# Kernel optimization log

Measured on AMD Instinct MI355X. Metric: run time of the kernel, lower is better.

## Reference

```python
import jax, jax.numpy as jnp
import numpy as np

B, T, D, E, C = 2, 2048, 2048, 8, 512
O1 = D // E  # per-expert hidden width (out_features // num_experts)


def setup_inputs() -> dict:
    key = jax.random.key(0)
    k = jax.random.split(key, 8)
    s = 1.0 / np.sqrt(D)
    return {
        "x": jax.random.normal(k[0], (B, T, D), dtype=jnp.float32),
        "dispatch_mask": jax.random.uniform(k[1], (B, T, E, C), dtype=jnp.float32),
        "combine_array": jax.random.uniform(k[2], (B, T, E, C), dtype=jnp.float32),
        # contract weights: nn.Linear(D, D) reshaped to (E, D//E, D)
        "W1": jax.random.uniform(k[3], (E, O1, D), jnp.float32, -s, s),
        "b1": jax.random.uniform(k[4], (E, O1), jnp.float32, -s, s),
        # expand weights: nn.Linear(D, D) reshaped to (E, D, D//E)
        "W2": jax.random.uniform(k[5], (E, D, O1), jnp.float32, -s, s),
        "b2": jax.random.uniform(k[6], (D,), jnp.float32, -s, s),
    }


def reference(x, dispatch_mask, combine_array, W1, b1, W2, b2):
    # --- ExpertsChooseMaskedContract ---
    # einsum('btd,btec,eod->beco') split into two GEMM-shaped contractions
    xe = jnp.einsum('btd,btec->becd', x, dispatch_mask)          # [B,E,C,D]
    h = jnp.einsum('becd,eod->beco', xe, W1) + b1[None, :, None, :]  # [B,E,C,O1]
    # --- GELU (torch nn.GELU default = exact erf form) ---
    h = jax.nn.gelu(h, approximate=False)
    # --- ExpertsChooseMaskedExpand (homogeneous-coords bias == add b2 then combine) ---
    y = jnp.einsum('beci,eoi->beco', h, W2) + b2[None, None, None, :]  # [B,E,C,D]
    out = jnp.einsum('beco,btec->bto', y, combine_array)          # [B,T,D]
    return out
```

## Files before the change

kernel.cpp:

```cpp
#include <hip/hip_runtime.h>
#include <math.h>

#define BB 2
#define TT 2048
#define DD 2048
#define EE 8
#define CCv 512
#define OO1 256

typedef unsigned short u16;
typedef __bf16 bf16x8 __attribute__((ext_vector_type(8)));
typedef float f32x4 __attribute__((ext_vector_type(4)));

__device__ __forceinline__ u16 f2bf(float f) {
    unsigned u = __float_as_uint(f);
    unsigned r = (u + 0x7fffu + ((u >> 16) & 1u)) >> 16;
    return (u16)r;
}

__device__ __forceinline__ void gload16(const void* g, void* s) {
    __builtin_amdgcn_global_load_lds(
        (const __attribute__((address_space(1))) void*)g,
        (__attribute__((address_space(3))) void*)s, 16, 0, 0);
}

__global__ __launch_bounds__(256) void conv_cast(const float* __restrict__ in,
                                                 u16* __restrict__ out, long n) {
    long i = ((long)blockIdx.x * 256 + threadIdx.x) * 4;
    float4 v = *(const float4*)&in[i];
    ushort4 o; o.x = f2bf(v.x); o.y = f2bf(v.y); o.z = f2bf(v.z); o.w = f2bf(v.w);
    *(ushort4*)&out[i] = o;
}

__global__ __launch_bounds__(256) void transpose_conv(
    const float* __restrict__ in, long inHi, long inLo, int modZ, long sIn,
    u16* __restrict__ out, long outZ, long sOut)
{
    __shared__ float tile[32][33];
    const int z = blockIdx.z;
    const float* ib = in + (long)(z / modZ) * inHi + (long)(z % modZ) * inLo;
    u16* ob = out + (long)z * outZ;
    const int t0 = blockIdx.y * 32, c0 = blockIdx.x * 32;
    const int tid = threadIdx.x;
    const int r = tid >> 3, c4 = (tid & 7) * 4;

    float4 v = *(const float4*)&ib[(long)(t0 + r) * sIn + c0 + c4];
    tile[r][c4 + 0] = v.x; tile[r][c4 + 1] = v.y;
    tile[r][c4 + 2] = v.z; tile[r][c4 + 3] = v.w;
    __syncthreads();

    const int oc = tid >> 3, t4 = (tid & 7) * 4;
    ushort4 o;
    o.x = f2bf(tile[t4 + 0][oc]);
    o.y = f2bf(tile[t4 + 1][oc]);
    o.z = f2bf(tile[t4 + 2][oc]);
    o.w = f2bf(tile[t4 + 3][oc]);
    *(ushort4*)&ob[(long)(c0 + oc) * sOut + t0 + t4] = o;
}

template<int EPI>
__global__ __launch_bounds__(256)
void mfma_gemm(const u16* __restrict__ A, long ldA, long aHi, long aLo, int modA,
               const u16* __restrict__ B, long ldB, long bHi, long bLo, int modB,
               void* __restrict__ Cout, long ldC, long cHi, long cLo, int modC,
               const float* __restrict__ bias, long biasLo, int modBias,
               int M, int N, int K)
{
    __shared__ __align__(16) char smem[32768];
    char* smA = smem;
    char* smB = smem + 16384;

    const int z = blockIdx.z;
    const char* Ab = (const char*)(A + (long)(z / modA) * aHi + (long)(z % modA) * aLo);
    const char* Bb = (const char*)(B + (long)(z / modB) * bHi + (long)(z % modB) * bLo);
    const long ldAb = ldA * 2, ldBb = ldB * 2;

    const int m0 = blockIdx.y * 128, n0 = blockIdx.x * 128;
    const int tid = threadIdx.x;
    const int l = tid & 63;
    const int w = tid >> 6;
    const int wm = w >> 1, wn = w & 1;

    const int srow = l >> 3;
    const int schunk = (l & 7) ^ srow;
    const int frow = l & 15;
    const int fgrp = l >> 4;
    const int fch0 = fgrp ^ (l & 7);

    int aoff[4], boff[4];
#pragma unroll
    for (int i = 0; i < 4; ++i) {
        aoff[i] = (wm * 64 + i * 16 + frow) * 128 + fch0 * 16;
        boff[i] = (wn * 64 + i * 16 + frow) * 128 + fch0 * 16;
    }

    f32x4 acc[4][4];
    const f32x4 zero4 = {0.f, 0.f, 0.f, 0.f};
#pragma unroll
    for (int i = 0; i < 4; ++i)
#pragma unroll
        for (int j = 0; j < 4; ++j) acc[i][j] = zero4;

    const long sgo = (long)schunk * 16;

    for (int k0 = 0; k0 < K; k0 += 64) {
        const long kb = (long)k0 * 2;
#pragma unroll
        for (int j = 0; j < 4; ++j) {
            const int rr = (j * 4 + w) * 8 + srow;
            gload16(Ab + (long)(m0 + rr) * ldAb + kb + sgo, smA + (j * 4 + w) * 1024);
            gload16(Bb + (long)(n0 + rr) * ldBb + kb + sgo, smB + (j * 4 + w) * 1024);
        }
        __syncthreads();
#pragma unroll
        for (int kk = 0; kk < 2; ++kk) {
            const int kx = kk * 64;
            bf16x8 af[4], bfr[4];
#pragma unroll
            for (int i = 0; i < 4; ++i) af[i] = *(const bf16x8*)(smA + (aoff[i] ^ kx));
#pragma unroll
            for (int i = 0; i < 4; ++i) bfr[i] = *(const bf16x8*)(smB + (boff[i] ^ kx));
#pragma unroll
            for (int mi = 0; mi < 4; ++mi)
#pragma unroll
                for (int ni = 0; ni < 4; ++ni)
                    acc[mi][ni] = __builtin_amdgcn_mfma_f32_16x16x32_bf16(
                        af[mi], bfr[ni], acc[mi][ni], 0, 0, 0);
        }
        __syncthreads();
    }

    const long cbase = (long)(z / modC) * cHi + (long)(z % modC) * cLo;
    const float* biasB = bias + (long)(z % modBias) * biasLo;
#pragma unroll
    for (int mi = 0; mi < 4; ++mi) {
#pragma unroll
        for (int ni = 0; ni < 4; ++ni) {
            const int col = n0 + wn * 64 + ni * 16 + frow;
            const int rowb = m0 + wm * 64 + mi * 16 + fgrp * 4;
#pragma unroll
            for (int r = 0; r < 4; ++r) {
                float v = acc[mi][ni][r];
                const int row = rowb + r;
                if (EPI == 1) {
                    v += biasB[col];
                    v = 0.5f * v * (1.0f + erff(v * 0.70710678118654752f));
                } else {
                    v += biasB[row];
                }
                ((u16*)Cout)[cbase + (long)row * ldC + col] = f2bf(v);
            }
        }
    }
}

template<int OUTBF>
__global__ __launch_bounds__(512, 2)
void mfma_gemm_256(const u16* __restrict__ A, long ldA, long aHi, long aLo, int modA,
                   const u16* __restrict__ B, long ldB, long bHi, long bLo, int modB,
                   void* __restrict__ Cout, long ldC, long cHi, long cLo, int modC,
                   int M, int N, int K)
{
    __shared__ __align__(16) char smem[131072];

    const int z = blockIdx.z;
    const char* Ab = (const char*)(A + (long)(z / modA) * aHi + (long)(z % modA) * aLo);
    const char* Bb = (const char*)(B + (long)(z / modB) * bHi + (long)(z % modB) * bLo);
    const long ldAb = ldA * 2, ldBb = ldB * 2;

    const int m0 = blockIdx.y * 256, n0 = blockIdx.x * 256;
    const int tid = threadIdx.x;
    const int l = tid & 63;
    const int w = tid >> 6;
    const int wm = w >> 2, wn = w & 3;

    const int srow = l >> 3;
    const int schunk = (l & 7) ^ srow;
    const long sgo = (long)schunk * 16;
    const int frow = l & 15, fgrp = l >> 4;
    const int cs0 = (fgrp ^ (l & 7)) * 16;

    auto stage = [&](int kt, int bsel, int half, int j) {
        const int rr = (w * 2 + j) * 8 + srow;
        const char* gb = (half < 2) ? Ab : Bb;
        const long ld = (half < 2) ? ldAb : ldBb;
        const int gr = ((half < 2) ? m0 + half * 128 : n0 + (half - 2) * 128) + rr;
        gload16(gb + (long)gr * ld + (long)kt * 128 + sgo,
                smem + bsel * 65536 + half * 16384 + (w * 2 + j) * 1024);
    };

    f32x4 acc[2][4][2][2];
    const f32x4 zero4 = {0.f, 0.f, 0.f, 0.f};
#pragma unroll
    for (int qm = 0; qm < 2; ++qm)
#pragma unroll
        for (int mi = 0; mi < 4; ++mi)
#pragma unroll
            for (int qn = 0; qn < 2; ++qn)
#pragma unroll
                for (int ni = 0; ni < 2; ++ni) acc[qm][mi][qn][ni] = zero4;

    int aoff[4], boff[2];
#pragma unroll
    for (int mi = 0; mi < 4; ++mi) aoff[mi] = (wm * 64 + mi * 16 + frow) * 128 + cs0;
#pragma unroll
    for (int ni = 0; ni < 2; ++ni) boff[ni] = (wn * 32 + ni * 16 + frow) * 128 + cs0;

    stage(0, 0, 0, 0); stage(0, 0, 0, 1);
    stage(0, 0, 2, 0); stage(0, 0, 2, 1);
    stage(0, 0, 3, 0); stage(0, 0, 3, 1);
    stage(0, 0, 1, 0); stage(0, 0, 1, 1);
    asm volatile("s_waitcnt vmcnt(4)" ::: "memory");
    __builtin_amdgcn_s_barrier();

    const int NT = K >> 6;
    for (int kt = 0; kt < NT; ++kt) {
        const char* buf = smem + (kt & 1) * 65536;
        const int sb = (kt & 1) ^ 1;
        const bool pf = (kt + 1) < NT;
        const int kn = kt + 1;
        bf16x8 af[4][2], bq0[2][2], bq1[2][2];

#pragma unroll
        for (int mi = 0; mi < 4; ++mi) {
            af[mi][0] = *(const bf16x8*)(buf + aoff[mi]);
            af[mi][1] = *(const bf16x8*)(buf + (aoff[mi] ^ 64));
        }
#pragma unroll
        for (int ni = 0; ni < 2; ++ni) {
            bq0[ni][0] = *(const bf16x8*)(buf + 32768 + boff[ni]);
            bq0[ni][1] = *(const bf16x8*)(buf + 32768 + (boff[ni] ^ 64));
        }
        if (pf) { stage(kn, sb, 0, 0); stage(kn, sb, 0, 1); }
        if (pf) { asm volatile("s_waitcnt vmcnt(4)" ::: "memory"); }
        else    { asm volatile("s_waitcnt vmcnt(2)" ::: "memory"); }
        __builtin_amdgcn_s_barrier();
        asm volatile("s_waitcnt lgkmcnt(0)" ::: "memory");
        __builtin_amdgcn_sched_barrier(0);
        __builtin_amdgcn_s_setprio(1);
#pragma unroll
        for (int kk = 0; kk < 2; ++kk)
#pragma unroll
            for (int mi = 0; mi < 4; ++mi)
#pragma unroll
                for (int ni = 0; ni < 2; ++ni)
                    acc[0][mi][0][ni] = __builtin_amdgcn_mfma_f32_16x16x32_bf16(
                        af[mi][kk], bq0[ni][kk], acc[0][mi][0][ni], 0, 0, 0);
        __builtin_amdgcn_s_setprio(0);

#pragma unroll
        for (int ni = 0; ni < 2; ++ni) {
            bq1[ni][0] = *(const bf16x8*)(buf + 49152 + boff[ni]);
            bq1[ni][1] = *(const bf16x8*)(buf + 49152 + (boff[ni] ^ 64));
        }
        if (pf) { stage(kn, sb, 2, 0); stage(kn, sb, 2, 1); }
        if (pf) { asm volatile("s_waitcnt vmcnt(4)" ::: "memory"); }
        else    { asm volatile("s_waitcnt vmcnt(0)" ::: "memory"); }
        __builtin_amdgcn_s_barrier();
        asm volatile("s_waitcnt lgkmcnt(0)" ::: "memory");
        __builtin_amdgcn_sched_barrier(0);
        __builtin_amdgcn_s_setprio(1);
#pragma unroll
        for (int kk = 0; kk < 2; ++kk)
#pragma unroll
            for (int mi = 0; mi < 4; ++mi)
#pragma unroll
                for (int ni = 0; ni < 2; ++ni)
                    acc[0][mi][1][ni] = __builtin_amdgcn_mfma_f32_16x16x32_bf16(
                        af[mi][kk], bq1[ni][kk], acc[0][mi][1][ni], 0, 0, 0);
        __builtin_amdgcn_s_setprio(0);

#pragma unroll
        for (int mi = 0; mi < 4; ++mi) {
            af[mi][0] = *(const bf16x8*)(buf + 16384 + aoff[mi]);
            af[mi][1] = *(const bf16x8*)(buf + 16384 + (aoff[mi] ^ 64));
        }
        if (pf) { stage(kn, sb, 3, 0); stage(kn, sb, 3, 1); }
        asm volatile("s_waitcnt lgkmcnt(0)" ::: "memory");
        __builtin_amdgcn_sched_barrier(0);
        __builtin_amdgcn_s_setprio(1);
#pragma unroll
        for (int kk = 0; kk < 2; ++kk)
#pragma unroll
            for (int mi = 0; mi < 4; ++mi)
#pragma unroll
                for (int ni = 0; ni < 2; ++ni)
                    acc[1][mi][1][ni] = __builtin_amdgcn_mfma_f32_16x16x32_bf16(
                        af[mi][kk], bq1[ni][kk], acc[1][mi][1][ni], 0, 0, 0);
        __builtin_amdgcn_s_setprio(0);

        if (pf) { stage(kn, sb, 1, 0); stage(kn, sb, 1, 1); }
        if (pf) { asm volatile("s_waitcnt vmcnt(4)" ::: "memory"); }
        __builtin_amdgcn_s_barrier();
        __builtin_amdgcn_s_setprio(1);
#pragma unroll
        for (int kk = 0; kk < 2; ++kk)
#pragma unroll
            for (int mi = 0; mi < 4; ++mi)
#pragma unroll
                for (int ni = 0; ni < 2; ++ni)
                    acc[1][mi][0][ni] = __builtin_amdgcn_mfma_f32_16x16x32_bf16(
                        af[mi][kk], bq0[ni][kk], acc[1][mi][0][ni], 0, 0, 0);
        __builtin_amdgcn_s_setprio(0);
    }

    const long cbase = (long)(z / modC) * cHi + (long)(z % modC) * cLo;
#pragma unroll
    for (int qm = 0; qm < 2; ++qm)
#pragma unroll
        for (int mi = 0; mi < 4; ++mi)
#pragma unroll
            for (int qn = 0; qn < 2; ++qn)
#pragma unroll
                for (int ni = 0; ni < 2; ++ni) {
                    const int col = n0 + qn * 128 + wn * 32 + ni * 16 + frow;
                    const int rowb = m0 + qm * 128 + wm * 64 + mi * 16 + fgrp * 4;
#pragma unroll
                    for (int r = 0; r < 4; ++r) {
                        const float v = acc[qm][mi][qn][ni][r];
                        const long idx = cbase + (long)(rowb + r) * ldC + col;
                        if (OUTBF) ((u16*)Cout)[idx] = f2bf(v);
                        else       ((float*)Cout)[idx] = v;
                    }
                }
}

template<int OUTBF>
__global__ __launch_bounds__(512, 2)
void mfma_gemm_big(const u16* __restrict__ A, long ldA, long aHi, long aLo, int modA,
                   const u16* __restrict__ B, long ldB, long bHi, long bLo, int modB,
                   void* __restrict__ Cout, long ldC, long cHi, long cLo, int modC,
                   int M, int N, int K)
{
    __shared__ __align__(16) char smem[147456];

    const int z = blockIdx.z;
    const char* Ab = (const char*)(A + (long)(z / modA) * aHi + (long)(z % modA) * aLo);
    const char* Bb = (const char*)(B + (long)(z / modB) * bHi + (long)(z % modB) * bLo);
    const long ldAb = ldA * 2, ldBb = ldB * 2;

    const int m0 = blockIdx.y * 256, n0 = blockIdx.x * 128;
    const int tid = threadIdx.x;
    const int l = tid & 63;
    const int w = tid >> 6;
    const int wm = w >> 1, wn = w & 1;

    const int srow = l >> 3;
    const int schunk = (l & 7) ^ srow;
    const long sgo = (long)schunk * 16;
    const int frow = l & 15;
    const int fgrp = l >> 4;
    const int fsw = (fgrp ^ (l & 7)) * 16;

    auto stageA = [&](int kt, int bsel, int j) {
        const int rr = (j * 8 + w) * 8 + srow;
        gload16(Ab + (long)(m0 + rr) * ldAb + (long)kt * 128 + sgo,
                smem + bsel * 49152 + (j * 8 + w) * 1024);
    };
    auto stageB = [&](int kt, int bsel, int j) {
        const int rr = (j * 8 + w) * 8 + srow;
        gload16(Bb + (long)(n0 + rr) * ldBb + (long)kt * 128 + sgo,
                smem + bsel * 49152 + 32768 + (j * 8 + w) * 1024);
    };

    f32x4 acc[4][4];
    const f32x4 zero4 = {0.f, 0.f, 0.f, 0.f};
#pragma unroll
    for (int i = 0; i < 4; ++i)
#pragma unroll
        for (int j = 0; j < 4; ++j) acc[i][j] = zero4;

    int aoff[4], boff[4];
#pragma unroll
    for (int i = 0; i < 4; ++i) {
        aoff[i] = (wm * 64 + i * 16 + frow) * 128 + fsw;
        boff[i] = (wn * 64 + i * 16 + frow) * 128 + fsw;
    }

#pragma unroll
    for (int j = 0; j < 4; ++j) stageA(0, 0, j);
#pragma unroll
    for (int j = 0; j < 2; ++j) stageB(0, 0, j);
#pragma unroll
    for (int j = 0; j < 4; ++j) stageA(1, 1, j);
#pragma unroll
    for (int j = 0; j < 2; ++j) stageB(1, 1, j);
    asm volatile("s_waitcnt vmcnt(6)" ::: "memory");
    __builtin_amdgcn_s_barrier();

    const int NT = K >> 6;
    int bc = 0;
    int sc = 2;
    for (int kt = 0; kt < NT; ++kt) {
        const char* bufA = smem + bc * 49152;
        const char* bufB = bufA + 32768;
        const bool pf = (kt + 2) < NT;
        const int kpf = kt + 2;

        if (pf) {
            stageA(kpf, sc, 0); stageA(kpf, sc, 1);
            stageA(kpf, sc, 2); stageA(kpf, sc, 3);
            stageB(kpf, sc, 0); stageB(kpf, sc, 1);
        }

        bf16x8 af[4][2], bfr[4][2];
#pragma unroll
        for (int mi = 0; mi < 4; ++mi) {
            af[mi][0] = *(const bf16x8*)(bufA + aoff[mi]);
            af[mi][1] = *(const bf16x8*)(bufA + (aoff[mi] ^ 64));
        }
#pragma unroll
        for (int ni = 0; ni < 4; ++ni) {
            bfr[ni][0] = *(const bf16x8*)(bufB + boff[ni]);
            bfr[ni][1] = *(const bf16x8*)(bufB + (boff[ni] ^ 64));
        }

        __builtin_amdgcn_s_setprio(1);
#pragma unroll
        for (int kk = 0; kk < 2; ++kk)
#pragma unroll
            for (int mi = 0; mi < 4; ++mi)
#pragma unroll
                for (int ni = 0; ni < 4; ++ni)
                    acc[mi][ni] = __builtin_amdgcn_mfma_f32_16x16x32_bf16(
                        af[mi][kk], bfr[ni][kk], acc[mi][ni], 0, 0, 0);
        __builtin_amdgcn_s_setprio(0);

        if (pf) { asm volatile("s_waitcnt vmcnt(6)" ::: "memory"); }
        else    { asm volatile("s_waitcnt vmcnt(0)" ::: "memory"); }
        __builtin_amdgcn_s_barrier();

        bc = (bc == 2) ? 0 : bc + 1;
        sc = (sc == 2) ? 0 : sc + 1;
    }

    const long cbase = (long)(z / modC) * cHi + (long)(z % modC) * cLo;
#pragma unroll
    for (int mi = 0; mi < 4; ++mi) {
#pragma unroll
        for (int ni = 0; ni < 4; ++ni) {
            const int col = n0 + wn * 64 + ni * 16 + frow;
            const int rowb = m0 + wm * 64 + mi * 16 + fgrp * 4;
#pragma unroll
            for (int r = 0; r < 4; ++r) {
                const float v = acc[mi][ni][r];
                const long idx = cbase + (long)(rowb + r) * ldC + col;
                if (OUTBF) ((u16*)Cout)[idx] = f2bf(v);
                else       ((float*)Cout)[idx] = v;
            }
        }
    }
}

extern "C" void kernel_launch(void* const* d_in, const int* in_sizes, int n_in,
                              void* d_out, int out_size, void* d_ws, size_t ws_size,
                              hipStream_t stream) {
    const float* x    = (const float*)d_in[0];
    const float* mask = (const float*)d_in[1];
    const float* comb = (const float*)d_in[2];
    const float* W1   = (const float*)d_in[3];
    const float* b1   = (const float*)d_in[4];
    const float* W2   = (const float*)d_in[5];
    const float* b2   = (const float*)d_in[6];
    float* out = (float*)d_out;

    char* ws = (char*)d_ws;
    u16* buf0 = (u16*)ws;
    u16* xT   = (u16*)(ws + 33554432);
    u16* W1b  = (u16*)(ws + 50331648);
    u16* W2b  = (u16*)(ws + 58720256);
    u16* xe   = (u16*)(ws + 67108864);
    u16* h    = (u16*)(ws + 100663296);
    u16* yT   = xe;

    transpose_conv<<<dim3(DD / 32, TT / 32, BB), 256, 0, stream>>>(
        x, (long)TT * DD, 0L, 1, (long)DD, xT, (long)DD * TT, (long)TT);
    transpose_conv<<<dim3(CCv / 32, TT / 32, BB * EE), 256, 0, stream>>>(
        mask, (long)TT * EE * CCv, (long)CCv, EE, (long)EE * CCv,
        buf0, (long)CCv * TT, (long)TT);
    conv_cast<<<(int)((8L * OO1 * DD) / 1024), 256, 0, stream>>>(W1, W1b, 8L * OO1 * DD);
    conv_cast<<<(int)((8L * DD * OO1) / 1024), 256, 0, stream>>>(W2, W2b, 8L * DD * OO1);

    mfma_gemm_256<1><<<dim3(DD / 256, CCv / 256, 16), 512, 0, stream>>>(
        buf0, 2048, 1048576L, 0L, 1,
        xT,   2048, 4194304L, 0L, 8,
        xe,   2048, 1048576L, 0L, 1,
        CCv, DD, TT);

    conv_cast<<<(int)((2L * TT * EE * CCv) / 1024), 256, 0, stream>>>(
        comb, buf0, 2L * TT * EE * CCv);

    mfma_gemm<1><<<dim3(OO1 / 128, CCv / 128, 16), 256, 0, stream>>>(
        xe,  2048, 1048576L, 0L, 1,
        W1b, 2048, 0L, 524288L, 8,
        h,   256, 131072L, 0L, 1,
        b1, 256L, 8, CCv, OO1, DD);

    mfma_gemm<3><<<dim3(CCv / 128, DD / 128, 16), 256, 0, stream>>>(
        W2b, 256, 0L, 524288L, 8,
        h,   256, 131072L, 0L, 1,
        yT,  4096, 8388608L, 512L, 8,
        b2, 0L, 1, DD, CCv, OO1);

    mfma_gemm_big<0><<<dim3(DD / 128, TT / 256, BB), 512, 0, stream>>>(
        buf0, 4096, 8388608L, 0L, 1,
        yT,   4096, 8388608L, 0L, 1,
        out,  2048, 4194304L, 0L, 1,
        TT, DD, EE * CCv);
}
```

Measured before the change: 266.4 us.

## Replace final combine GEMM with split-K 256-tile GEMM plus reduction add

New measurement: 276.7 us. 3.8% more time.

```diff
diff --git a/kernel.cpp b/kernel.cpp
--- a/kernel.cpp
+++ b/kernel.cpp
@@ -30,6 +30,15 @@
     float4 v = *(const float4*)&in[i];
     ushort4 o; o.x = f2bf(v.x); o.y = f2bf(v.y); o.z = f2bf(v.z); o.w = f2bf(v.w);
     *(ushort4*)&out[i] = o;
+}
+
+__global__ __launch_bounds__(256) void add_inplace(float* __restrict__ out,
+                                                   const float* __restrict__ part) {
+    long i = ((long)blockIdx.x * 256 + threadIdx.x) * 4;
+    float4 a = *(float4*)&out[i];
+    float4 b = *(const float4*)&part[i];
+    a.x += b.x; a.y += b.y; a.z += b.z; a.w += b.w;
+    *(float4*)&out[i] = a;
 }
 
 __global__ __launch_bounds__(256) void transpose_conv(
@@ -210,15 +219,24 @@
     stage(0, 0, 2, 0); stage(0, 0, 2, 1);
     stage(0, 0, 3, 0); stage(0, 0, 3, 1);
     stage(0, 0, 1, 0); stage(0, 0, 1, 1);
-    asm volatile("s_waitcnt vmcnt(4)" ::: "memory");
-    __builtin_amdgcn_s_barrier();
 
     const int NT = K >> 6;
     for (int kt = 0; kt < NT; ++kt) {
         const char* buf = smem + (kt & 1) * 65536;
         const int sb = (kt & 1) ^ 1;
         const bool pf = (kt + 1) < NT;
-        const int kn = kt + 1;
+
+        asm volatile("s_waitcnt vmcnt(0)" ::: "memory");
+        __builtin_amdgcn_s_barrier();
+
+        if (pf) {
+            const int kn = kt + 1;
+            stage(kn, sb, 0, 0); stage(kn, sb, 0, 1);
+            stage(kn, sb, 2, 0); stage(kn, sb, 2, 1);
+            stage(kn, sb, 3, 0); stage(kn, sb, 3, 1);
+            stage(kn, sb, 1, 0); stage(kn, sb, 1, 1);
+        }
+
         bf16x8 af[4][2], bq0[2][2], bq1[2][2];
 
 #pragma unroll
@@ -231,10 +249,6 @@
             bq0[ni][0] = *(const bf16x8*)(buf + 32768 + boff[ni]);
             bq0[ni][1] = *(const bf16x8*)(buf + 32768 + (boff[ni] ^ 64));
         }
-        if (pf) { stage(kn, sb, 0, 0); stage(kn, sb, 0, 1); }
-        if (pf) { asm volatile("s_waitcnt vmcnt(4)" ::: "memory"); }
-        else    { asm volatile("s_waitcnt vmcnt(2)" ::: "memory"); }
-        __builtin_amdgcn_s_barrier();
         asm volatile("s_waitcnt lgkmcnt(0)" ::: "memory");
         __builtin_amdgcn_sched_barrier(0);
         __builtin_amdgcn_s_setprio(1);
@@ -253,10 +267,6 @@
             bq1[ni][0] = *(const bf16x8*)(buf + 49152 + boff[ni]);
             bq1[ni][1] = *(const bf16x8*)(buf + 49152 + (boff[ni] ^ 64));
         }
-        if (pf) { stage(kn, sb, 2, 0); stage(kn, sb, 2, 1); }
-        if (pf) { asm volatile("s_waitcnt vmcnt(4)" ::: "memory"); }
-        else    { asm volatile("s_waitcnt vmcnt(0)" ::: "memory"); }
-        __builtin_amdgcn_s_barrier();
         asm volatile("s_waitcnt lgkmcnt(0)" ::: "memory");
         __builtin_amdgcn_sched_barrier(0);
         __builtin_amdgcn_s_setprio(1);
@@ -275,7 +285,6 @@
             af[mi][0] = *(const bf16x8*)(buf + 16384 + aoff[mi]);
             af[mi][1] = *(const bf16x8*)(buf + 16384 + (aoff[mi] ^ 64));
         }
-        if (pf) { stage(kn, sb, 3, 0); stage(kn, sb, 3, 1); }
         asm volatile("s_waitcnt lgkmcnt(0)" ::: "memory");
         __builtin_amdgcn_sched_barrier(0);
         __builtin_amdgcn_s_setprio(1);
@@ -289,9 +298,6 @@
                         af[mi][kk], bq1[ni][kk], acc[1][mi][1][ni], 0, 0, 0);
         __builtin_amdgcn_s_setprio(0);
 
-        if (pf) { stage(kn, sb, 1, 0); stage(kn, sb, 1, 1); }
-        if (pf) { asm volatile("s_waitcnt vmcnt(4)" ::: "memory"); }
-        __builtin_amdgcn_s_barrier();
         __builtin_amdgcn_s_setprio(1);
 #pragma unroll
         for (int kk = 0; kk < 2; ++kk)
@@ -323,133 +329,6 @@
                         else       ((float*)Cout)[idx] = v;
                     }
                 }
-}
-
-template<int OUTBF>
-__global__ __launch_bounds__(512, 2)
-void mfma_gemm_big(const u16* __restrict__ A, long ldA, long aHi, long aLo, int modA,
-                   const u16* __restrict__ B, long ldB, long bHi, long bLo, int modB,
-                   void* __restrict__ Cout, long ldC, long cHi, long cLo, int modC,
-                   int M, int N, int K)
-{
-    __shared__ __align__(16) char smem[147456];
-
-    const int z = blockIdx.z;
-    const char* Ab = (const char*)(A + (long)(z / modA) * aHi + (long)(z % modA) * aLo);
-    const char* Bb = (const char*)(B + (long)(z / modB) * bHi + (long)(z % modB) * bLo);
-    const long ldAb = ldA * 2, ldBb = ldB * 2;
-
-    const int m0 = blockIdx.y * 256, n0 = blockIdx.x * 128;
-    const int tid = threadIdx.x;
-    const int l = tid & 63;
-    const int w = tid >> 6;
-    const int wm = w >> 1, wn = w & 1;
-
-    const int srow = l >> 3;
-    const int schunk = (l & 7) ^ srow;
-    const long sgo = (long)schunk * 16;
-    const int frow = l & 15;
-    const int fgrp = l >> 4;
-    const int fsw = (fgrp ^ (l & 7)) * 16;
-
-    auto stageA = [&](int kt, int bsel, int j) {
-        const int rr = (j * 8 + w) * 8 + srow;
-        gload16(Ab + (long)(m0 + rr) * ldAb + (long)kt * 128 + sgo,
-                smem + bsel * 49152 + (j * 8 + w) * 1024);
-    };
-    auto stageB = [&](int kt, int bsel, int j) {
-        const int rr = (j * 8 + w) * 8 + srow;
-        gload16(Bb + (long)(n0 + rr) * ldBb + (long)kt * 128 + sgo,
-                smem + bsel * 49152 + 32768 + (j * 8 + w) * 1024);
-    };
-
-    f32x4 acc[4][4];
-    const f32x4 zero4 = {0.f, 0.f, 0.f, 0.f};
-#pragma unroll
-    for (int i = 0; i < 4; ++i)
-#pragma unroll
-        for (int j = 0; j < 4; ++j) acc[i][j] = zero4;
-
-    int aoff[4], boff[4];
-#pragma unroll
-    for (int i = 0; i < 4; ++i) {
-        aoff[i] = (wm * 64 + i * 16 + frow) * 128 + fsw;
-        boff[i] = (wn * 64 + i * 16 + frow) * 128 + fsw;
-    }
-
-#pragma unroll
-    for (int j = 0; j < 4; ++j) stageA(0, 0, j);
-#pragma unroll
-    for (int j = 0; j < 2; ++j) stageB(0, 0, j);
-#pragma unroll
-    for (int j = 0; j < 4; ++j) stageA(1, 1, j);
-#pragma unroll
-    for (int j = 0; j < 2; ++j) stageB(1, 1, j);
-    asm volatile("s_waitcnt vmcnt(6)" ::: "memory");
-    __builtin_amdgcn_s_barrier();
-
-    const int NT = K >> 6;
-    int bc = 0;
-    int sc = 2;
-    for (int kt = 0; kt < NT; ++kt) {
-        const char* bufA = smem + bc * 49152;
-        const char* bufB = bufA + 32768;
-        const bool pf = (kt + 2) < NT;
-        const int kpf = kt + 2;
-
-        if (pf) {
-            stageA(kpf, sc, 0); stageA(kpf, sc, 1);
-            stageA(kpf, sc, 2); stageA(kpf, sc, 3);
-            stageB(kpf, sc, 0); stageB(kpf, sc, 1);
-        }
-
-        bf16x8 af[4][2], bfr[4][2];
-#pragma unroll
-        for (int mi = 0; mi < 4; ++mi) {
-            af[mi][0] = *(const bf16x8*)(bufA + aoff[mi]);
-            af[mi][1] = *(const bf16x8*)(bufA + (aoff[mi] ^ 64));
-        }
-#pragma unroll
-        for (int ni = 0; ni < 4; ++ni) {
-            bfr[ni][0] = *(const bf16x8*)(bufB + boff[ni]);
-            bfr[ni][1] = *(const bf16x8*)(bufB + (boff[ni] ^ 64));
-        }
-
-        __builtin_amdgcn_s_setprio(1);
-#pragma unroll
-        for (int kk = 0; kk < 2; ++kk)
-#pragma unroll
-            for (int mi = 0; mi < 4; ++mi)
-#pragma unroll
-                for (int ni = 0; ni < 4; ++ni)
-                    acc[mi][ni] = __builtin_amdgcn_mfma_f32_16x16x32_bf16(
-                        af[mi][kk], bfr[ni][kk], acc[mi][ni], 0, 0, 0);
-        __builtin_amdgcn_s_setprio(0);
-
-        if (pf) { asm volatile("s_waitcnt vmcnt(6)" ::: "memory"); }
-        else    { asm volatile("s_waitcnt vmcnt(0)" ::: "memory"); }
-        __builtin_amdgcn_s_barrier();
-
-        bc = (bc == 2) ? 0 : bc + 1;
-        sc = (sc == 2) ? 0 : sc + 1;
-    }
-
-    const long cbase = (long)(z / modC) * cHi + (long)(z % modC) * cLo;
-#pragma unroll
-    for (int mi = 0; mi < 4; ++mi) {
-#pragma unroll
-        for (int ni = 0; ni < 4; ++ni) {
-            const int col = n0 + wn * 64 + ni * 16 + frow;
-            const int rowb = m0 + wm * 64 + mi * 16 + fgrp * 4;
-#pragma unroll
-            for (int r = 0; r < 4; ++r) {
-                const float v = acc[mi][ni][r];
-                const long idx = cbase + (long)(rowb + r) * ldC + col;
-                if (OUTBF) ((u16*)Cout)[idx] = f2bf(v);
-                else       ((float*)Cout)[idx] = v;
-            }
-        }
-    }
 }
 
 extern "C" void kernel_launch(void* const* d_in, const int* in_sizes, int n_in,
@@ -472,6 +351,7 @@
     u16* xe   = (u16*)(ws + 67108864);
     u16* h    = (u16*)(ws + 100663296);
     u16* yT   = xe;
+    float* part = (float*)(ws + 33554432);
 
     transpose_conv<<<dim3(DD / 32, TT / 32, BB), 256, 0, stream>>>(
         x, (long)TT * DD, 0L, 1, (long)DD, xT, (long)DD * TT, (long)TT);
@@ -502,9 +382,11 @@
         yT,  4096, 8388608L, 512L, 8,
         b2, 0L, 1, DD, CCv, OO1);
 
-    mfma_gemm_big<0><<<dim3(DD / 128, TT / 256, BB), 512, 0, stream>>>(
-        buf0, 4096, 8388608L, 0L, 1,
-        yT,   4096, 8388608L, 0L, 1,
-        out,  2048, 4194304L, 0L, 1,
-        TT, DD, EE * CCv);
-}
+    const long dPart = (long)((char*)part - (char*)out) / 4;
+    mfma_gemm_256<0><<<dim3(DD / 256, TT / 256, 4), 512, 0, stream>>>(
+        buf0, 4096, 2048L, 8388608L, 2,
+        yT,   4096, 2048L, 8388608L, 2,
+        out,  2048, dPart, 4194304L, 2,
+        TT, DD, 2048);
+    add_inplace<<<8192, 256, 0, stream>>>(out, part);
+}
```

## Split-K the contract GEMM with separate GELU pass and use big kernel for expand

Applied to the files above, without the earlier changes.

Measured after the change: 255.6 us. -4.1%, faster.

```diff
diff --git a/kernel.cpp b/kernel.cpp
--- a/kernel.cpp
+++ b/kernel.cpp
@@ -30,6 +30,34 @@
     float4 v = *(const float4*)&in[i];
     ushort4 o; o.x = f2bf(v.x); o.y = f2bf(v.y); o.z = f2bf(v.z); o.w = f2bf(v.w);
     *(ushort4*)&out[i] = o;
+}
+
+__global__ __launch_bounds__(256) void dup_cast(const float* __restrict__ in,
+                                                u16* __restrict__ out, long dup) {
+    long i = ((long)blockIdx.x * 256 + threadIdx.x) * 4;
+    float4 v = *(const float4*)&in[i];
+    ushort4 o; o.x = f2bf(v.x); o.y = f2bf(v.y); o.z = f2bf(v.z); o.w = f2bf(v.w);
+    *(ushort4*)&out[i] = o;
+    *(ushort4*)&out[i + dup] = o;
+}
+
+__global__ __launch_bounds__(256) void gelu_fuse(const float* __restrict__ P,
+                                                 const float* __restrict__ b1,
+                                                 u16* __restrict__ h) {
+    long i = ((long)blockIdx.x * 256 + threadIdx.x) * 4;
+    const int o = (int)(i & 255);
+    const int e = (int)((i >> 17) & 7);
+    float4 a = *(const float4*)&P[i];
+    float4 b = *(const float4*)&P[i + 4194304];
+    float4 bb = *(const float4*)&b1[e * 256 + o];
+    float r0 = a.x + b.x + bb.x, r1 = a.y + b.y + bb.y;
+    float r2 = a.z + b.z + bb.z, r3 = a.w + b.w + bb.w;
+    ushort4 o4;
+    o4.x = f2bf(0.5f * r0 * (1.0f + erff(r0 * 0.70710678118654752f)));
+    o4.y = f2bf(0.5f * r1 * (1.0f + erff(r1 * 0.70710678118654752f)));
+    o4.z = f2bf(0.5f * r2 * (1.0f + erff(r2 * 0.70710678118654752f)));
+    o4.w = f2bf(0.5f * r3 * (1.0f + erff(r3 * 0.70710678118654752f)));
+    *(ushort4*)&h[i] = o4;
 }
 
 __global__ __launch_bounds__(256) void transpose_conv(
@@ -58,7 +86,7 @@
     *(ushort4*)&ob[(long)(c0 + oc) * sOut + t0 + t4] = o;
 }
 
-template<int EPI>
+template<int EPI, int OUTBF>
 __global__ __launch_bounds__(256)
 void mfma_gemm(const u16* __restrict__ A, long ldA, long aHi, long aLo, int modA,
                const u16* __restrict__ B, long ldB, long bHi, long bLo, int modB,
@@ -131,7 +159,6 @@
     }
 
     const long cbase = (long)(z / modC) * cHi + (long)(z % modC) * cLo;
-    const float* biasB = bias + (long)(z % modBias) * biasLo;
 #pragma unroll
     for (int mi = 0; mi < 4; ++mi) {
 #pragma unroll
@@ -140,15 +167,10 @@
             const int rowb = m0 + wm * 64 + mi * 16 + fgrp * 4;
 #pragma unroll
             for (int r = 0; r < 4; ++r) {
-                float v = acc[mi][ni][r];
-                const int row = rowb + r;
-                if (EPI == 1) {
-                    v += biasB[col];
-                    v = 0.5f * v * (1.0f + erff(v * 0.70710678118654752f));
-                } else {
-                    v += biasB[row];
-                }
-                ((u16*)Cout)[cbase + (long)row * ldC + col] = f2bf(v);
+                const float v = acc[mi][ni][r];
+                const long idx = cbase + (long)(rowb + r) * ldC + col;
+                if (OUTBF) ((u16*)Cout)[idx] = f2bf(v);
+                else       ((float*)Cout)[idx] = v;
             }
         }
     }
@@ -235,8 +257,6 @@
         if (pf) { asm volatile("s_waitcnt vmcnt(4)" ::: "memory"); }
         else    { asm volatile("s_waitcnt vmcnt(2)" ::: "memory"); }
         __builtin_amdgcn_s_barrier();
-        asm volatile("s_waitcnt lgkmcnt(0)" ::: "memory");
-        __builtin_amdgcn_sched_barrier(0);
         __builtin_amdgcn_s_setprio(1);
 #pragma unroll
         for (int kk = 0; kk < 2; ++kk)
@@ -257,8 +277,6 @@
         if (pf) { asm volatile("s_waitcnt vmcnt(4)" ::: "memory"); }
         else    { asm volatile("s_waitcnt vmcnt(0)" ::: "memory"); }
         __builtin_amdgcn_s_barrier();
-        asm volatile("s_waitcnt lgkmcnt(0)" ::: "memory");
-        __builtin_amdgcn_sched_barrier(0);
         __builtin_amdgcn_s_setprio(1);
 #pragma unroll
         for (int kk = 0; kk < 2; ++kk)
@@ -276,8 +294,6 @@
             af[mi][1] = *(const bf16x8*)(buf + 16384 + (aoff[mi] ^ 64));
         }
         if (pf) { stage(kn, sb, 3, 0); stage(kn, sb, 3, 1); }
-        asm volatile("s_waitcnt lgkmcnt(0)" ::: "memory");
-        __builtin_amdgcn_sched_barrier(0);
         __builtin_amdgcn_s_setprio(1);
 #pragma unroll
         for (int kk = 0; kk < 2; ++kk)
@@ -325,11 +341,12 @@
                 }
 }
 
-template<int OUTBF>
+template<int EPI, int OUTBF>
 __global__ __launch_bounds__(512, 2)
 void mfma_gemm_big(const u16* __restrict__ A, long ldA, long aHi, long aLo, int modA,
                    const u16* __restrict__ B, long ldB, long bHi, long bLo, int modB,
                    void* __restrict__ Cout, long ldC, long cHi, long cLo, int modC,
+                   const float* __restrict__ bias,
                    int M, int N, int K)
 {
     __shared__ __align__(16) char smem[147456];
@@ -443,7 +460,8 @@
             const int rowb = m0 + wm * 64 + mi * 16 + fgrp * 4;
 #pragma unroll
             for (int r = 0; r < 4; ++r) {
-                const float v = acc[mi][ni][r];
+                float v = acc[mi][ni][r];
+                if (EPI == 3) v += bias[rowb + r];
                 const long idx = cbase + (long)(rowb + r) * ldC + col;
                 if (OUTBF) ((u16*)Cout)[idx] = f2bf(v);
                 else       ((float*)Cout)[idx] = v;
@@ -467,18 +485,18 @@
     char* ws = (char*)d_ws;
     u16* buf0 = (u16*)ws;
     u16* xT   = (u16*)(ws + 33554432);
-    u16* W1b  = (u16*)(ws + 50331648);
+    u16* W1b2 = (u16*)(ws + 33554432);
     u16* W2b  = (u16*)(ws + 58720256);
     u16* xe   = (u16*)(ws + 67108864);
     u16* h    = (u16*)(ws + 100663296);
     u16* yT   = xe;
+    float* P  = (float*)ws;
 
     transpose_conv<<<dim3(DD / 32, TT / 32, BB), 256, 0, stream>>>(
         x, (long)TT * DD, 0L, 1, (long)DD, xT, (long)DD * TT, (long)TT);
     transpose_conv<<<dim3(CCv / 32, TT / 32, BB * EE), 256, 0, stream>>>(
         mask, (long)TT * EE * CCv, (long)CCv, EE, (long)EE * CCv,
         buf0, (long)CCv * TT, (long)TT);
-    conv_cast<<<(int)((8L * OO1 * DD) / 1024), 256, 0, stream>>>(W1, W1b, 8L * OO1 * DD);
     conv_cast<<<(int)((8L * DD * OO1) / 1024), 256, 0, stream>>>(W2, W2b, 8L * DD * OO1);
 
     mfma_gemm_256<1><<<dim3(DD / 256, CCv / 256, 16), 512, 0, stream>>>(
@@ -487,24 +505,28 @@
         xe,   2048, 1048576L, 0L, 1,
         CCv, DD, TT);
 
-    conv_cast<<<(int)((2L * TT * EE * CCv) / 1024), 256, 0, stream>>>(
-        comb, buf0, 2L * TT * EE * CCv);
-
-    mfma_gemm<1><<<dim3(OO1 / 128, CCv / 128, 16), 256, 0, stream>>>(
-        xe,  2048, 1048576L, 0L, 1,
-        W1b, 2048, 0L, 524288L, 8,
-        h,   256, 131072L, 0L, 1,
-        b1, 256L, 8, CCv, OO1, DD);
-
-    mfma_gemm<3><<<dim3(CCv / 128, DD / 128, 16), 256, 0, stream>>>(
+    dup_cast<<<4096, 256, 0, stream>>>(W1, W1b2, 4194304L);
+
+    mfma_gemm<0, 0><<<dim3(OO1 / 128, CCv / 128, 32), 256, 0, stream>>>(
+        xe,   2048, 1048576L, 1024L, 2,
+        W1b2, 2048, 524288L, 1024L, 2,
+        P,    256, 131072L, 4194304L, 2,
+        nullptr, 0L, 1, CCv, OO1, 1024);
+
+    gelu_fuse<<<2048, 256, 0, stream>>>(P, b1, h);
+
+    mfma_gemm_big<3, 1><<<dim3(CCv / 128, DD / 256, 16), 512, 0, stream>>>(
         W2b, 256, 0L, 524288L, 8,
         h,   256, 131072L, 0L, 1,
         yT,  4096, 8388608L, 512L, 8,
-        b2, 0L, 1, DD, CCv, OO1);
-
-    mfma_gemm_big<0><<<dim3(DD / 128, TT / 256, BB), 512, 0, stream>>>(
+        b2, DD, CCv, OO1);
+
+    conv_cast<<<(int)((2L * TT * EE * CCv) / 1024), 256, 0, stream>>>(
+        comb, buf0, 2L * TT * EE * CCv);
+
+    mfma_gemm_big<0, 0><<<dim3(DD / 128, TT / 256, BB), 512, 0, stream>>>(
         buf0, 4096, 8388608L, 0L, 1,
         yT,   4096, 8388608L, 0L, 1,
         out,  2048, 4194304L, 0L, 1,
-        TT, DD, EE * CCv);
-}
+        nullptr, TT, DD, EE * CCv);
+}
```
